# Performance work log

Measured on AMD Instinct MI355X. Metric: run time of the kernel, lower is better.

## Reference

```python
import jax, jax.numpy as jnp
import numpy as np

D = 3       # in_out_dim
HID = 64    # hidden_dim
WIDTH = 64  # planar flow width
BATCH = 500000
BLOCK = D * WIDTH  # 192


def setup_inputs() -> dict:
    key = jax.random.key(0)
    ks = jax.random.split(key, 9)
    s1 = 1.0                      # fan_in=1
    s2 = 1.0 / np.sqrt(HID)
    return {
        "t": jax.random.uniform(ks[0], (1,), dtype=jnp.float32),
        "z": jax.random.normal(ks[1], (BATCH, D), dtype=jnp.float32),
        "logp_z": jnp.zeros((BATCH, 1), dtype=jnp.float32),
        "fc1_w": jax.random.normal(ks[2], (HID, 1), dtype=jnp.float32) * s1,
        "fc1_b": jax.random.normal(ks[3], (HID,), dtype=jnp.float32) * s1,
        "fc2_w": jax.random.normal(ks[4], (HID, HID), dtype=jnp.float32) * s2,
        "fc2_b": jax.random.normal(ks[5], (HID,), dtype=jnp.float32) * s2,
        "fc3_w": jax.random.normal(ks[6], (3 * BLOCK + WIDTH, HID), dtype=jnp.float32) * s2,
        "fc3_b": jax.random.normal(ks[7], (3 * BLOCK + WIDTH,), dtype=jnp.float32) * s2,
    }


def _hypernet(t, fc1_w, fc1_b, fc2_w, fc2_b, fc3_w, fc3_b):
    p = t.reshape(1, 1)
    p = jnp.tanh(p @ fc1_w.T + fc1_b)
    p = jnp.tanh(p @ fc2_w.T + fc2_b)
    p = (p @ fc3_w.T + fc3_b).reshape(-1)          # [3*BLOCK + WIDTH]
    W = p[:BLOCK].reshape(WIDTH, D)                # w_k vectors
    U = p[BLOCK:2 * BLOCK].reshape(WIDTH, D)
    G = p[2 * BLOCK:3 * BLOCK].reshape(WIDTH, D)
    U = U * jax.nn.sigmoid(G)                      # gated u_k vectors
    B = p[3 * BLOCK:]                              # [WIDTH] biases
    return W, B, U


def reference(t, z, logp_z, fc1_w, fc1_b, fc2_w, fc2_b, fc3_w, fc3_b):
    W, B, U = _hypernet(t, fc1_w, fc1_b, fc2_w, fc2_b, fc3_w, fc3_b)
    # h_k(z) = tanh(z . w_k + b_k)  -> [BATCH, WIDTH]
    h = jnp.tanh(z @ W.T + B)
    # dz/dt = mean_k h_k * u_k -> [BATCH, D]
    dz_dt = (h @ U) / WIDTH
    # trace of d(dz_dt)/dz, closed form: mean_k (1 - h_k^2) * (w_k . u_k)
    wu = jnp.sum(W * U, axis=1)                    # [WIDTH]
    trace = ((1.0 - h * h) @ wu) / WIDTH           # [BATCH]
    dlogp_z_dt = -trace[:, None]                   # [BATCH, 1]
    return dz_dt, dlogp_z_dt
```

## Files before the change

### kernel.cpp

```cpp
#include <hip/hip_runtime.h>
#include <math.h>

#define D      3
#define HID    64
#define WIDTH  64
#define BATCH  500000
#define BLOCKP (D * WIDTH)
#define NPAR   (3 * BLOCKP + WIDTH)
#define NPAIR  (BATCH / 2)

typedef float f2 __attribute__((ext_vector_type(2)));

__device__ __forceinline__ f2 sp(float s) { f2 r; r.x = s; r.y = s; return r; }
__device__ __forceinline__ f2 vfma(f2 a, f2 b, f2 c) {
    return __builtin_elementwise_fma(a, b, c);
}

__global__ __launch_bounds__(256) void hyper_kernel(
    const float* __restrict__ t,
    const float* __restrict__ fc1_w, const float* __restrict__ fc1_b,
    const float* __restrict__ fc2_w, const float* __restrict__ fc2_b,
    const float* __restrict__ fc3_w, const float* __restrict__ fc3_b,
    float4* __restrict__ par)
{
    __shared__ float p1[HID];
    __shared__ float p2[HID];
    __shared__ float p3[NPAR];

    const int tid = threadIdx.x;

    if (tid < HID) {
        p1[tid] = tanhf(t[0] * fc1_w[tid] + fc1_b[tid]);
    }
    __syncthreads();
    if (tid < HID) {
        const float* wrow = fc2_w + tid * HID;
        float a0 = 0.f, a1 = 0.f, a2 = 0.f, a3 = 0.f;
        #pragma unroll
        for (int k = 0; k < HID; k += 4) {
            a0 = fmaf(wrow[k + 0], p1[k + 0], a0);
            a1 = fmaf(wrow[k + 1], p1[k + 1], a1);
            a2 = fmaf(wrow[k + 2], p1[k + 2], a2);
            a3 = fmaf(wrow[k + 3], p1[k + 3], a3);
        }
        p2[tid] = tanhf(((a0 + a1) + (a2 + a3)) + fc2_b[tid]);
    }
    __syncthreads();
    for (int o = tid; o < NPAR; o += blockDim.x) {
        float acc = fc3_b[o];
        const float4* w4 = (const float4*)(fc3_w + o * HID);
        const float4* q4 = (const float4*)p2;
        #pragma unroll
        for (int k = 0; k < HID / 4; ++k) {
            float4 w = w4[k];
            float4 q = q4[k];
            acc += w.x * q.x + w.y * q.y + w.z * q.z + w.w * q.w;
        }
        p3[o] = acc;
    }
    __syncthreads();
    if (tid < WIDTH) {
        float W0 = p3[3 * tid + 0], W1 = p3[3 * tid + 1], W2 = p3[3 * tid + 2];
        float U0 = p3[BLOCKP + 3 * tid + 0], U1 = p3[BLOCKP + 3 * tid + 1], U2 = p3[BLOCKP + 3 * tid + 2];
        float G0 = p3[2 * BLOCKP + 3 * tid + 0], G1 = p3[2 * BLOCKP + 3 * tid + 1], G2 = p3[2 * BLOCKP + 3 * tid + 2];
        float B  = p3[3 * BLOCKP + tid];
        U0 *= 1.0f / (1.0f + expf(-G0));
        U1 *= 1.0f / (1.0f + expf(-G1));
        U2 *= 1.0f / (1.0f + expf(-G2));
        float wu = W0 * U0 + W1 * U1 + W2 * U2;
        const float c = 2.8853900817779268f;
        const float s = 1.0f / (float)WIDTH;
        par[tid]         = make_float4(W0 * c, W1 * c, W2 * c, B * c);
        par[WIDTH + tid] = make_float4(U0 * s, U1 * s, U2 * s, -wu * s);
    }
}

__global__ __launch_bounds__(256) void cnf_main(
    const float* __restrict__ z,
    const float4* __restrict__ par,
    float* __restrict__ out)
{
    __shared__ float4 stab[2 * WIDTH];

    const int tid = threadIdx.x;
    if (tid < 2 * WIDTH) stab[tid] = par[tid];
    __syncthreads();

    const int gid = blockIdx.x * blockDim.x + tid;
    if (gid >= NPAIR) return;

    const f2* zp = (const f2*)z + (size_t)gid * 3;
    f2 v0 = zp[0], v1 = zp[1], v2 = zp[2];
    f2 z0 = {v0.x, v1.y};
    f2 z1 = {v0.y, v2.x};
    f2 z2 = {v1.x, v2.y};

    f2 dz0 = sp(0.f), dz1 = sp(0.f), dz2 = sp(0.f), tr = sp(0.f);

    const float4* sA = stab;
    const float4* sB = stab + WIDTH;

    #pragma unroll 8
    for (int j = 0; j < WIDTH; ++j) {
        float4 a = sA[j];
        float4 b = sB[j];

        f2 x = vfma(z0, sp(a.x), vfma(z1, sp(a.y), vfma(z2, sp(a.z), sp(a.w))));
        x = __builtin_elementwise_min(x, sp(30.0f));

        f2 d;
        d.x = __builtin_amdgcn_exp2f(x.x);
        d.y = __builtin_amdgcn_exp2f(x.y);
        d = d + sp(1.0f);

        float R = __builtin_amdgcn_rcpf(d.x * d.y);
        f2 inv; inv.x = R * d.y; inv.y = R * d.x;

        f2 h  = vfma(sp(-2.0f), inv, sp(1.0f));
        f2 g1 = vfma(-h, h, sp(1.0f));

        dz0 = vfma(h,  sp(b.x), dz0);
        dz1 = vfma(h,  sp(b.y), dz1);
        dz2 = vfma(h,  sp(b.z), dz2);
        tr  = vfma(g1, sp(b.w), tr);
    }

    f2* o = (f2*)out + (size_t)gid * 3;
    f2 w0 = {dz0.x, dz1.x};
    f2 w1 = {dz2.x, dz0.y};
    f2 w2 = {dz1.y, dz2.y};
    o[0] = w0; o[1] = w1; o[2] = w2;

    ((f2*)(out + 3 * BATCH))[gid] = tr;
}

extern "C" void kernel_launch(void* const* d_in, const int* in_sizes, int n_in,
                              void* d_out, int out_size, void* d_ws, size_t ws_size,
                              hipStream_t stream) {
    const float* t     = (const float*)d_in[0];
    const float* z     = (const float*)d_in[1];
    const float* fc1_w = (const float*)d_in[3];
    const float* fc1_b = (const float*)d_in[4];
    const float* fc2_w = (const float*)d_in[5];
    const float* fc2_b = (const float*)d_in[6];
    const float* fc3_w = (const float*)d_in[7];
    const float* fc3_b = (const float*)d_in[8];
    float* out = (float*)d_out;

    float4* par = (float4*)d_ws;

    hyper_kernel<<<1, 256, 0, stream>>>(
        t, fc1_w, fc1_b, fc2_w, fc2_b, fc3_w, fc3_b, par);

    const int threads = 256;
    const int blocks  = (NPAIR + threads - 1) / threads;
    cnf_main<<<blocks, threads, 0, stream>>>(z, par, out);
}
```

Baseline: 94.13 us.

## Parallelize hypernetwork across 64 blocks, one per planar flow unit

The single-block hypernetwork kernel is split into 64 blocks of 64 threads. Each block recomputes the small fc1/fc2 layers and then evaluates only the 10 fc3 rows it needs for its flow unit k. This spreads the serial fc3 matrix-vector work, which was done by one block, across many compute units, at the cost of computing the first two layers redundantly in every block.

```diff
diff --git a/kernel.cpp b/kernel.cpp
--- a/kernel.cpp
+++ b/kernel.cpp
@@ -16,7 +16,7 @@
     return __builtin_elementwise_fma(a, b, c);
 }
 
-__global__ __launch_bounds__(256) void hyper_kernel(
+__global__ __launch_bounds__(64) void hyper_kernel(
     const float* __restrict__ t,
     const float* __restrict__ fc1_w, const float* __restrict__ fc1_b,
     const float* __restrict__ fc2_w, const float* __restrict__ fc2_b,
@@ -25,15 +25,14 @@
 {
     __shared__ float p1[HID];
     __shared__ float p2[HID];
-    __shared__ float p3[NPAR];
+    __shared__ float q[16];
 
     const int tid = threadIdx.x;
+    const int tb  = blockIdx.x;
 
-    if (tid < HID) {
-        p1[tid] = tanhf(t[0] * fc1_w[tid] + fc1_b[tid]);
-    }
+    p1[tid] = tanhf(t[0] * fc1_w[tid] + fc1_b[tid]);
     __syncthreads();
-    if (tid < HID) {
+    {
         const float* wrow = fc2_w + tid * HID;
         float a0 = 0.f, a1 = 0.f, a2 = 0.f, a3 = 0.f;
         #pragma unroll
@@ -46,32 +45,34 @@
         p2[tid] = tanhf(((a0 + a1) + (a2 + a3)) + fc2_b[tid]);
     }
     __syncthreads();
-    for (int o = tid; o < NPAR; o += blockDim.x) {
-        float acc = fc3_b[o];
-        const float4* w4 = (const float4*)(fc3_w + o * HID);
+    if (tid < 10) {
+        const int row = (tid < 9) ? ((tid / 3) * BLOCKP + 3 * tb + (tid % 3))
+                                  : (3 * BLOCKP + tb);
+        const float4* w4 = (const float4*)(fc3_w + (size_t)row * HID);
         const float4* q4 = (const float4*)p2;
+        float acc = fc3_b[row];
         #pragma unroll
         for (int k = 0; k < HID / 4; ++k) {
             float4 w = w4[k];
-            float4 q = q4[k];
-            acc += w.x * q.x + w.y * q.y + w.z * q.z + w.w * q.w;
+            float4 p = q4[k];
+            acc += w.x * p.x + w.y * p.y + w.z * p.z + w.w * p.w;
         }
-        p3[o] = acc;
+        q[tid] = acc;
     }
     __syncthreads();
-    if (tid < WIDTH) {
-        float W0 = p3[3 * tid + 0], W1 = p3[3 * tid + 1], W2 = p3[3 * tid + 2];
-        float U0 = p3[BLOCKP + 3 * tid + 0], U1 = p3[BLOCKP + 3 * tid + 1], U2 = p3[BLOCKP + 3 * tid + 2];
-        float G0 = p3[2 * BLOCKP + 3 * tid + 0], G1 = p3[2 * BLOCKP + 3 * tid + 1], G2 = p3[2 * BLOCKP + 3 * tid + 2];
-        float B  = p3[3 * BLOCKP + tid];
+    if (tid == 0) {
+        float W0 = q[0], W1 = q[1], W2 = q[2];
+        float U0 = q[3], U1 = q[4], U2 = q[5];
+        float G0 = q[6], G1 = q[7], G2 = q[8];
+        float B  = q[9];
         U0 *= 1.0f / (1.0f + expf(-G0));
         U1 *= 1.0f / (1.0f + expf(-G1));
         U2 *= 1.0f / (1.0f + expf(-G2));
         float wu = W0 * U0 + W1 * U1 + W2 * U2;
         const float c = 2.8853900817779268f;
         const float s = 1.0f / (float)WIDTH;
-        par[tid]         = make_float4(W0 * c, W1 * c, W2 * c, B * c);
-        par[WIDTH + tid] = make_float4(U0 * s, U1 * s, U2 * s, -wu * s);
+        par[tb]         = make_float4(W0 * c, W1 * c, W2 * c, B * c);
+        par[WIDTH + tb] = make_float4(U0 * s, U1 * s, U2 * s, -wu * s);
     }
 }
 
@@ -149,7 +150,7 @@
 
     float4* par = (float4*)d_ws;
 
-    hyper_kernel<<<1, 256, 0, stream>>>(
+    hyper_kernel<<<64, 64, 0, stream>>>(
         t, fc1_w, fc1_b, fc2_w, fc2_b, fc3_w, fc3_b, par);
 
     const int threads = 256;
```

Result: no change. 92.65 us (-1.6%).
